# Kernel tuning notes

Measured on AMD Instinct MI355X. Metric: run time of the kernel, lower is better.

The kernel has to match this reference:

```python
import jax, jax.numpy as jnp
import numpy as np

N = 80000   # nodes
E = 320000  # directed edges
B = 3200    # graphs (25 nodes each)
D = 256     # emb_dim
L = 5       # num_layer
SIZES = [121, 8, 12, 15, 10, 9, 7, 3, 3]          # atom-feature vocab sizes
ESIZES = [25, 6, 2]                               # bond-feature vocab sizes
OFFS = np.concatenate([[0], np.cumsum(SIZES)[:-1]])  # offsets into fused node table
BN_EPS = 1e-5


def setup_inputs() -> dict:
    key = jax.random.key(0)
    ks = jax.random.split(key, 32)
    # int node features, per-column vocab bound
    x = jnp.stack([jax.random.randint(ks[i], (N,), 0, SIZES[i]) for i in range(9)], axis=1)
    edge_index = jax.random.randint(ks[9], (2, E), 0, N)
    edge_attr = jnp.stack([jax.random.randint(ks[10 + j], (E,), 0, ESIZES[j]) for j in range(3)], axis=1)
    batch = jnp.arange(N) // (N // B)  # sorted graph ids, 25 nodes per graph
    s = 0.1
    node_emb = jax.random.normal(ks[13], (int(sum(SIZES)), D)) * s  # fused 9 tables
    edge_emb1 = jax.random.normal(ks[14], (L, 25, D)) * s
    edge_emb2 = jax.random.normal(ks[15], (L, 6, D)) * s
    edge_emb3 = jax.random.normal(ks[16], (L, 2, D)) * s
    w = 0.05
    W1 = jax.random.normal(ks[17], (L, D, 2 * D)) * w
    b1 = jnp.zeros((L, 2 * D))
    W2 = jax.random.normal(ks[18], (L, 2 * D, D)) * w
    b2 = jnp.zeros((L, D))
    bn_g = jnp.ones((L, D))
    bn_b = jnp.zeros((L, D))
    H = D // 2
    HW1 = jax.random.normal(ks[19], (D, H)) * w
    Hb1 = jnp.zeros((H,))
    HW2 = jax.random.normal(ks[20], (H, H)) * w
    Hb2 = jnp.zeros((H,))
    HW3 = jax.random.normal(ks[21], (H, 2)) * w
    Hb3 = jnp.zeros((2,))
    return {"x": x, "edge_index": edge_index, "edge_attr": edge_attr, "batch": batch,
            "node_emb": node_emb, "edge_emb1": edge_emb1, "edge_emb2": edge_emb2,
            "edge_emb3": edge_emb3, "W1": W1, "b1": b1, "W2": W2, "b2": b2,
            "bn_g": bn_g, "bn_b": bn_b, "HW1": HW1, "Hb1": Hb1, "HW2": HW2,
            "Hb2": Hb2, "HW3": HW3, "Hb3": Hb3}


def _gnn_graphpred(x, edge_index, edge_attr, batch, node_emb, edge_emb1, edge_emb2,
                   edge_emb3, W1, b1, W2, b2, bn_g, bn_b, HW1, Hb1, HW2, Hb2, HW3, Hb3):
    n = x.shape[0]
    offs = jnp.asarray(OFFS, dtype=x.dtype)
    # sum of 9 atom embeddings == one gather into fused table
    h = node_emb[x + offs[None, :]].sum(axis=1)            # [N, D]
    # add self loops; self-loop edge_attr = [22, 0, 0]
    loop = jnp.arange(n, dtype=edge_index.dtype)
    src = jnp.concatenate([edge_index[0], loop])
    dst = jnp.concatenate([edge_index[1], loop])
    ea0 = jnp.concatenate([edge_attr[:, 0], jnp.full((n,), 22, edge_attr.dtype)])
    ea1 = jnp.concatenate([edge_attr[:, 1], jnp.zeros((n,), edge_attr.dtype)])
    ea2 = jnp.concatenate([edge_attr[:, 2], jnp.zeros((n,), edge_attr.dtype)])
    nl = W1.shape[0]
    relu_flag = jnp.arange(nl) < (nl - 1)   # ReLU on all but last layer (JK='last')

    def layer(hc, p):
        e1, e2, e3, w1, bb1, w2, bb2, g, b, flag = p
        eemb = e1[ea0] + e2[ea1] + e3[ea2]                 # [E+N, D]
        msg = hc[src] + eemb                                # gather + add
        aggr = jax.ops.segment_sum(msg, dst, num_segments=n)  # scatter-sum
        h2 = jax.nn.relu(aggr @ w1 + bb1) @ w2 + bb2        # GIN MLP
        mean = h2.mean(axis=0)
        var = h2.var(axis=0)                                # BatchNorm (batch stats)
        h2 = (h2 - mean) * jax.lax.rsqrt(var + BN_EPS) * g + b
        h2 = jnp.where(flag, jax.nn.relu(h2), h2)
        return h2, None

    h, _ = jax.lax.scan(layer, h, (edge_emb1, edge_emb2, edge_emb3, W1, b1, W2, b2,
                                   bn_g, bn_b, relu_flag))
    # super_node_rep: last node of each graph (batch is sorted)
    last_idx = jax.ops.segment_max(jnp.arange(n), batch, num_segments=B)
    super_rep = h[last_idx]                                 # [B, D]
    z = jax.nn.elu(super_rep @ HW1 + Hb1)
    z = jax.nn.elu(z @ HW2 + Hb2)
    return z @ HW3 + Hb3                                    # [B, 2]


def reference(x, edge_index, edge_attr, batch, node_emb, edge_emb1, edge_emb2,
              edge_emb3, W1, b1, W2, b2, bn_g, bn_b, HW1, Hb1, HW2, Hb2, HW3, Hb3):
    return _gnn_graphpred(x, edge_index, edge_attr, batch, node_emb, edge_emb1,
                          edge_emb2, edge_emb3, W1, b1, W2, b2, bn_g, bn_b,
                          HW1, Hb1, HW2, Hb2, HW3, Hb3)
```

## Files before the change

### kernel.cpp

```cpp
#include <hip/hip_runtime.h>
#include <hip/hip_bf16.h>

#define NN 80000
#define EE 320000
#define ET 400000
#define BB 3200
#define LL 5
#define NBLK 313
#define MLPB 1250

typedef __attribute__((ext_vector_type(8))) short bf16x8;
typedef __attribute__((ext_vector_type(8))) unsigned short u16x8;
typedef __attribute__((ext_vector_type(4))) float f32x4;

__device__ __forceinline__ float bf2f(unsigned short u) {
    unsigned int v = ((unsigned int)u) << 16;
    return __builtin_bit_cast(float, v);
}
__device__ __forceinline__ unsigned short f2bf(float f) {
    return __builtin_bit_cast(unsigned short, __float2bfloat16(f));
}

#define GLL16(SRC, DST) __builtin_amdgcn_global_load_lds( \
    (const __attribute__((address_space(1))) unsigned int*)(SRC), \
    (__attribute__((address_space(3))) unsigned int*)(DST), 16, 0, 0)


__global__ void k_deg(const int* ei, int* deg) {
    int e = blockIdx.x * 256 + threadIdx.x;
    if (e >= ET) return;
    int d = (e < EE) ? ei[EE + e] : (e - EE);
    atomicAdd(&deg[d], 1);
}

__global__ void k_scan1(const int* deg, int* blksum) {
    __shared__ int sh[256];
    int t = threadIdx.x, b = blockIdx.x;
    int i = b * 256 + t;
    int v = (i < NN) ? deg[i] : 0;
    sh[t] = v; __syncthreads();
    for (int off = 128; off > 0; off >>= 1) {
        if (t < off) sh[t] += sh[t + off];
        __syncthreads();
    }
    if (t == 0) blksum[b] = sh[0];
}

__global__ __launch_bounds__(512) void k_scan2(const int* blksum, int* blkoff) {
    __shared__ int sh[512];
    int t = threadIdx.x;
    int v = (t < NBLK) ? blksum[t] : 0;
    sh[t] = v; __syncthreads();
    for (int off = 1; off < 512; off <<= 1) {
        int x = (t >= off) ? sh[t - off] : 0;
        __syncthreads();
        sh[t] += x;
        __syncthreads();
    }
    if (t < NBLK) blkoff[t] = sh[t] - v;
}

__global__ void k_scan3(const int* deg, const int* blkoff, int* row_start, int* cursor) {
    __shared__ int sh[256];
    int t = threadIdx.x, b = blockIdx.x;
    int i = b * 256 + t;
    int v = (i < NN) ? deg[i] : 0;
    sh[t] = v; __syncthreads();
    for (int off = 1; off < 256; off <<= 1) {
        int x = (t >= off) ? sh[t - off] : 0;
        __syncthreads();
        sh[t] += x;
        __syncthreads();
    }
    int exc = sh[t] - v + blkoff[b];
    if (i < NN) { row_start[i] = exc; cursor[i] = exc; }
    if (i == NN - 1) row_start[NN] = exc + v;
}

__global__ void k_fill(const int* ei, const int* ea, int* cursor, int* eid, int* combo) {
    int e = blockIdx.x * 256 + threadIdx.x;
    if (e >= ET) return;
    int d = (e < EE) ? ei[EE + e] : (e - EE);
    int p = atomicAdd(&cursor[d], 1);
    eid[p] = e;
    int c;
    if (e < EE) c = ea[e * 3 + 0] * 12 + ea[e * 3 + 1] * 2 + ea[e * 3 + 2];
    else        c = 22 * 12;
    combo[e] = c;
}

__global__ void k_sortbkt(const int* row_start, int* eid) {
    int v = blockIdx.x * 256 + threadIdx.x;
    if (v >= NN) return;
    int s0 = row_start[v], s1 = row_start[v + 1];
    for (int i = s0 + 1; i < s1; i++) {
        int key = eid[i];
        int j = i - 1;
        while (j >= s0 && eid[j] > key) { eid[j + 1] = eid[j]; j--; }
        eid[j + 1] = key;
    }
}

__global__ void k_remap(const int* eid, const int* combo, const int* ei_src,
                        int* csrc, int* ccomb) {
    int p = blockIdx.x * 256 + threadIdx.x;
    if (p >= ET) return;
    int e = eid[p];
    csrc[p]  = (e < EE) ? ei_src[e] : (e - EE);
    ccomb[p] = combo[e];
}

__global__ void k_ecomb(const float* e1, const float* e2, const float* e3, float* ec) {
    int l = blockIdx.x / 300, c = blockIdx.x % 300, d = threadIdx.x;
    int a0 = c / 12, a1 = (c / 2) % 6, a2 = c & 1;
    ec[(size_t)(l * 300 + c) * 256 + d] =
        e1[(size_t)(l * 25 + a0) * 256 + d] +
        e2[(size_t)(l * 6 + a1) * 256 + d] +
        e3[(size_t)(l * 2 + a2) * 256 + d];
}

__global__ void k_w1t(const float* W, __hip_bfloat16* Whi, __hip_bfloat16* Wlo) {
    int i = blockIdx.x * 256 + threadIdx.x;
    if (i >= LL * 512 * 256) return;
    int l = i / (512 * 256); int r = i % (512 * 256); int n = r / 256; int k = r % 256;
    float w = W[(size_t)(l * 256 + k) * 512 + n];
    unsigned short hi = f2bf(w);
    Whi[i] = __float2bfloat16(w);
    Wlo[i] = __float2bfloat16(w - bf2f(hi));
}
__global__ void k_w2t(const float* W, __hip_bfloat16* Whi, __hip_bfloat16* Wlo) {
    int i = blockIdx.x * 256 + threadIdx.x;
    if (i >= LL * 256 * 512) return;
    int l = i / (256 * 512); int r = i % (256 * 512); int n = r / 512; int k = r % 512;
    float w = W[(size_t)(l * 512 + k) * 256 + n];
    unsigned short hi = f2bf(w);
    Whi[i] = __float2bfloat16(w);
    Wlo[i] = __float2bfloat16(w - bf2f(hi));
}

__global__ void k_nodeemb(const int* x, const float* emb, __hip_bfloat16* h) {
    const int offs[9] = {0, 121, 129, 141, 156, 166, 175, 182, 185};
    int i = blockIdx.x; int d = threadIdx.x;
    float acc = 0.f;
#pragma unroll
    for (int c = 0; c < 9; c++) {
        int idx = x[i * 9 + c] + offs[c];
        acc += emb[(size_t)idx * 256 + d];
    }
    h[(size_t)i * 256 + d] = __float2bfloat16(acc);
}


__global__ __launch_bounds__(256) void k_aggr(const __hip_bfloat16* h, const float* ecomb_l,
        const int* row_start, const int* csrc, const int* ccomb,
        __hip_bfloat16* aggrB) {
    int wid = threadIdx.x >> 6;
    int lane = threadIdx.x & 63;
    int v = blockIdx.x * 8 + wid * 2 + (lane >> 5);
    int sl = lane & 31;
    int s0 = row_start[v], s1 = row_start[v + 1];
    const unsigned short* hp = (const unsigned short*)h;
    float acc[8] = {0.f, 0.f, 0.f, 0.f, 0.f, 0.f, 0.f, 0.f};
    int p = s0;
    for (; p + 2 <= s1; p += 2) {
        int sA = csrc[p],     cA = ccomb[p];
        int sB = csrc[p + 1], cB = ccomb[p + 1];
        u16x8 hA = *(const u16x8*)(hp + (size_t)sA * 256 + sl * 8);
        u16x8 hB = *(const u16x8*)(hp + (size_t)sB * 256 + sl * 8);
        f32x4 eA0 = *(const f32x4*)(ecomb_l + (size_t)cA * 256 + sl * 8);
        f32x4 eA1 = *(const f32x4*)(ecomb_l + (size_t)cA * 256 + sl * 8 + 4);
        f32x4 eB0 = *(const f32x4*)(ecomb_l + (size_t)cB * 256 + sl * 8);
        f32x4 eB1 = *(const f32x4*)(ecomb_l + (size_t)cB * 256 + sl * 8 + 4);
        float tA[8] = { bf2f(hA[0]) + eA0.x, bf2f(hA[1]) + eA0.y,
                        bf2f(hA[2]) + eA0.z, bf2f(hA[3]) + eA0.w,
                        bf2f(hA[4]) + eA1.x, bf2f(hA[5]) + eA1.y,
                        bf2f(hA[6]) + eA1.z, bf2f(hA[7]) + eA1.w };
        float tB[8] = { bf2f(hB[0]) + eB0.x, bf2f(hB[1]) + eB0.y,
                        bf2f(hB[2]) + eB0.z, bf2f(hB[3]) + eB0.w,
                        bf2f(hB[4]) + eB1.x, bf2f(hB[5]) + eB1.y,
                        bf2f(hB[6]) + eB1.z, bf2f(hB[7]) + eB1.w };
#pragma unroll
        for (int j = 0; j < 8; j++) { acc[j] += tA[j]; acc[j] += tB[j]; }
    }
    if (p < s1) {
        int s = csrc[p], c = ccomb[p];
        u16x8 hv = *(const u16x8*)(hp + (size_t)s * 256 + sl * 8);
        f32x4 e0 = *(const f32x4*)(ecomb_l + (size_t)c * 256 + sl * 8);
        f32x4 e1 = *(const f32x4*)(ecomb_l + (size_t)c * 256 + sl * 8 + 4);
        acc[0] += bf2f(hv[0]) + e0.x;
        acc[1] += bf2f(hv[1]) + e0.y;
        acc[2] += bf2f(hv[2]) + e0.z;
        acc[3] += bf2f(hv[3]) + e0.w;
        acc[4] += bf2f(hv[4]) + e1.x;
        acc[5] += bf2f(hv[5]) + e1.y;
        acc[6] += bf2f(hv[6]) + e1.z;
        acc[7] += bf2f(hv[7]) + e1.w;
    }
    u16x8 o;
#pragma unroll
    for (int j = 0; j < 8; j++) o[j] = f2bf(acc[j]);
    *(u16x8*)((unsigned short*)aggrB + (size_t)v * 256 + sl * 8) = o;
}

template<bool LAST>
__global__ __launch_bounds__(512) void k_mlp(const __hip_bfloat16* aggrB,
        const __hip_bfloat16* W1hi, const __hip_bfloat16* W1lo, const float* b1v,
        const __hip_bfloat16* W2hi, const __hip_bfloat16* W2lo, const float* b2v,
        float* h2, float* psum, float* psq) {
    __shared__ __align__(16) char smem[160 * 1024];
    int tid = threadIdx.x;
    int wave = tid >> 6, lane = tid & 63;
    int lr = lane & 15, lk = lane >> 4;
    int mBase = blockIdx.x * 64;

    {
        const char* srcBase = (const char*)aggrB + (size_t)mBase * 512;
#pragma unroll
        for (int i = 0; i < 4; i++) {
            int g0 = wave * 4096 + i * 1024;
            int flat = g0 + lane * 16;
            int r = flat >> 9;
            int slot = (flat >> 4) & 31;
            int srcf = (r << 9) | (((slot ^ (r & 7)) & 31) << 4);
            GLL16(srcBase + srcf, smem + g0);
        }
    }

    const char* W1hB = (const char*)W1hi;
    const char* W1lB = (const char*)W1lo;
    auto stageW1 = [&](int buf, int k0) {
        char* dst = smem + 32768 + buf * 65536;
#pragma unroll
        for (int i = 0; i < 4; i++) {
            int g0 = i * 512 + wave * 64;
            int g  = g0 + lane;
            int n = g >> 2, j = g & 3;
            int ks = j ^ ((n + (n >> 2)) & 3);
            size_t so = (size_t)n * 512 + (size_t)k0 * 2 + ks * 16;
            GLL16(W1hB + so, dst + g0 * 16);
            GLL16(W1lB + so, dst + 32768 + g0 * 16);
        }
    };

    stageW1(0, 0);
    __syncthreads();

    f32x4 acc1[4][4] = {};
    for (int t = 0; t < 8; t++) {
        int cur = t & 1;
        if (t + 1 < 8) stageW1(cur ^ 1, (t + 1) * 32);
        const char* bW = smem + 32768 + cur * 65536;
        bf16x8 wh[4], wl[4], a[4];
#pragma unroll
        for (int n = 0; n < 4; n++) {
            int n0 = wave * 64 + n * 16 + lr;
            int go = (n0 * 4 + (lk ^ ((n0 + (n0 >> 2)) & 3))) * 16;
            wh[n] = *(const bf16x8*)(bW + go);
            wl[n] = *(const bf16x8*)(bW + 32768 + go);
        }
#pragma unroll
        for (int m = 0; m < 4; m++) {
            int r = m * 16 + lr;
            a[m] = *(const bf16x8*)(smem + r * 512 + ((((t * 4 + lk) ^ (r & 7)) & 31) * 16));
        }
#pragma unroll
        for (int m = 0; m < 4; m++)
#pragma unroll
            for (int n = 0; n < 4; n++) {
                acc1[m][n] = __builtin_amdgcn_mfma_f32_16x16x32_bf16(wh[n], a[m], acc1[m][n], 0, 0, 0);
                acc1[m][n] = __builtin_amdgcn_mfma_f32_16x16x32_bf16(wl[n], a[m], acc1[m][n], 0, 0, 0);
            }
        __syncthreads();
    }

    short* sAct = (short*)smem;
#pragma unroll
    for (int n = 0; n < 4; n++) {
        int col0 = wave * 64 + n * 16 + lk * 4;
        f32x4 bi = *(const f32x4*)(b1v + col0);
        int cb = col0 >> 3, ci = col0 & 7;
#pragma unroll
        for (int m = 0; m < 4; m++) {
            int row = m * 16 + lr;
            short4 o;
            o.x = (short)f2bf(fmaxf(acc1[m][n][0] + bi.x, 0.f));
            o.y = (short)f2bf(fmaxf(acc1[m][n][1] + bi.y, 0.f));
            o.z = (short)f2bf(fmaxf(acc1[m][n][2] + bi.z, 0.f));
            o.w = (short)f2bf(fmaxf(acc1[m][n][3] + bi.w, 0.f));
            *(short4*)(&sAct[row * 512 + (((cb ^ (row & 7)) << 3) | ci)]) = o;
        }
    }

    const char* W2hB = (const char*)W2hi;
    const char* W2lB = (const char*)W2lo;
    auto stageW2 = [&](int buf, int k0) {
        char* dst = smem + 65536 + buf * 32768;
#pragma unroll
        for (int i = 0; i < 2; i++) {
            int g0 = i * 512 + wave * 64;
            int g  = g0 + lane;
            int n = g >> 2, j = g & 3;
            int ks = j ^ ((n + (n >> 2)) & 3);
            size_t so = (size_t)n * 1024 + (size_t)k0 * 2 + ks * 16;
            GLL16(W2hB + so, dst + g0 * 16);
            GLL16(W2lB + so, dst + 16384 + g0 * 16);
        }
    };
    stageW2(0, 0);
    __syncthreads();

    f32x4 acc2[4][2] = {};
    for (int t = 0; t < 16; t++) {
        int cur = t & 1;
        if (t + 1 < 16) stageW2(cur ^ 1, (t + 1) * 32);
        const char* bW = smem + 65536 + cur * 32768;
        bf16x8 a2[4], w2h[2], w2l[2];
        int kb = t * 4 + lk;
#pragma unroll
        for (int m = 0; m < 4; m++) {
            int row = m * 16 + lr;
            a2[m] = *(const bf16x8*)((const char*)sAct + row * 1024 + (((kb ^ (row & 7)) & 63) << 4));
        }
#pragma unroll
        for (int n = 0; n < 2; n++) {
            int n0 = wave * 32 + n * 16 + lr;
            int go = (n0 * 4 + (lk ^ ((n0 + (n0 >> 2)) & 3))) * 16;
            w2h[n] = *(const bf16x8*)(bW + go);
            w2l[n] = *(const bf16x8*)(bW + 16384 + go);
        }
#pragma unroll
        for (int m = 0; m < 4; m++)
#pragma unroll
            for (int n = 0; n < 2; n++) {
                acc2[m][n] = __builtin_amdgcn_mfma_f32_16x16x32_bf16(a2[m], w2h[n], acc2[m][n], 0, 0, 0);
                acc2[m][n] = __builtin_amdgcn_mfma_f32_16x16x32_bf16(a2[m], w2l[n], acc2[m][n], 0, 0, 0);
            }
        __syncthreads();
    }

    float colS[2] = {0.f, 0.f}, colQ[2] = {0.f, 0.f};
#pragma unroll
    for (int m = 0; m < 4; m++)
#pragma unroll
        for (int n = 0; n < 2; n++) {
            int col = wave * 32 + n * 16 + lr;
            float bi = b2v[col];
#pragma unroll
            for (int j = 0; j < 4; j++) {
                int row = mBase + m * 16 + lk * 4 + j;
                float v = acc2[m][n][j] + bi;
                colS[n] += v; colQ[n] += v * v;
                if (!LAST || (row % 25 == 24))
                    h2[(size_t)row * 256 + col] = v;
            }
        }
#pragma unroll
    for (int n = 0; n < 2; n++) {
        colS[n] += __shfl_xor(colS[n], 16);
        colQ[n] += __shfl_xor(colQ[n], 16);
        colS[n] += __shfl_xor(colS[n], 32);
        colQ[n] += __shfl_xor(colQ[n], 32);
    }
    if (lk == 0) {
#pragma unroll
        for (int n = 0; n < 2; n++) {
            int col = wave * 32 + n * 16 + lr;
            psum[(size_t)col * MLPB + blockIdx.x] = colS[n];
            psq [(size_t)col * MLPB + blockIdx.x] = colQ[n];
        }
    }
}

__global__ __launch_bounds__(256) void k_bn2(const float* psum, const float* psq,
                                             const float* g, const float* bta, float* stat) {
    __shared__ float s1[256], s2[256];
    int d = blockIdx.x; int t = threadIdx.x;
    float a = 0.f, b = 0.f;
    for (int rb = t; rb < MLPB; rb += 256) {
        a += psum[(size_t)d * MLPB + rb];
        b += psq [(size_t)d * MLPB + rb];
    }
    s1[t] = a; s2[t] = b; __syncthreads();
    for (int off = 128; off > 0; off >>= 1) {
        if (t < off) { s1[t] += s1[t + off]; s2[t] += s2[t + off]; }
        __syncthreads();
    }
    if (t == 0) {
        float mean = s1[0] / NN;
        float var = s2[0] / NN - mean * mean;
        float sc = rsqrtf(var + 1e-5f) * g[d];
        stat[d] = sc;
        stat[256 + d] = bta[d] - mean * sc;
    }
}

__global__ void k_bnapply(const float* h2, const float* stat, __hip_bfloat16* h, int relu) {
    int i = (blockIdx.x * 256 + threadIdx.x) * 4;
    int d = i & 255;
    f32x4 v = *(const f32x4*)(h2 + i);
    f32x4 sc = *(const f32x4*)(stat + d);
    f32x4 sh = *(const f32x4*)(stat + 256 + d);
    float r0 = v.x * sc.x + sh.x;
    float r1 = v.y * sc.y + sh.y;
    float r2 = v.z * sc.z + sh.z;
    float r3 = v.w * sc.w + sh.w;
    if (relu) {
        r0 = fmaxf(r0, 0.f); r1 = fmaxf(r1, 0.f);
        r2 = fmaxf(r2, 0.f); r3 = fmaxf(r3, 0.f);
    }
    ushort4 o;
    o.x = f2bf(r0); o.y = f2bf(r1); o.z = f2bf(r2); o.w = f2bf(r3);
    *(ushort4*)((unsigned short*)h + i) = o;
}

__global__ __launch_bounds__(128) void k_head(const float* h2, const float* stat,
        const float* HW1, const float* Hb1, const float* HW2, const float* Hb2,
        const float* HW3, const float* Hb3, float* out) {
    __shared__ float row[256], z1[128], z2[128];
    int g = blockIdx.x; int t = threadIdx.x;
    size_t node = (size_t)g * 25 + 24;
    row[t]       = h2[node * 256 + t] * stat[t] + stat[256 + t];
    row[t + 128] = h2[node * 256 + t + 128] * stat[t + 128] + stat[256 + t + 128];
    __syncthreads();
    float acc = Hb1[t];
    for (int k = 0; k < 256; k++) acc += row[k] * HW1[k * 128 + t];
    z1[t] = acc > 0.f ? acc : expm1f(acc);
    __syncthreads();
    acc = Hb2[t];
    for (int k = 0; k < 128; k++) acc += z1[k] * HW2[k * 128 + t];
    z2[t] = acc > 0.f ? acc : expm1f(acc);
    __syncthreads();
    if (t < 2) {
        acc = Hb3[t];
        for (int k = 0; k < 128; k++) acc += z2[k] * HW3[k * 2 + t];
        out[g * 2 + t] = acc;
    }
}


extern "C" void kernel_launch(void* const* d_in, const int* in_sizes, int n_in,
                              void* d_out, int out_size, void* d_ws, size_t ws_size,
                              hipStream_t stream) {
    const int* x          = (const int*)d_in[0];
    const int* edge_index = (const int*)d_in[1];
    const int* edge_attr  = (const int*)d_in[2];
    const float* node_emb = (const float*)d_in[4];
    const float* ee1 = (const float*)d_in[5];
    const float* ee2 = (const float*)d_in[6];
    const float* ee3 = (const float*)d_in[7];
    const float* W1  = (const float*)d_in[8];
    const float* b1  = (const float*)d_in[9];
    const float* W2  = (const float*)d_in[10];
    const float* b2  = (const float*)d_in[11];
    const float* bng = (const float*)d_in[12];
    const float* bnb = (const float*)d_in[13];
    const float* HW1 = (const float*)d_in[14];
    const float* Hb1 = (const float*)d_in[15];
    const float* HW2 = (const float*)d_in[16];
    const float* Hb2 = (const float*)d_in[17];
    const float* HW3 = (const float*)d_in[18];
    const float* Hb3 = (const float*)d_in[19];
    float* out = (float*)d_out;

    char* ws = (char*)d_ws;
    size_t off = 0;
    auto alloc = [&](size_t bytes) -> char* {
        off = (off + 255) & ~(size_t)255;
        char* p = ws + off;
        off += bytes;
        return p;
    };
    int* deg       = (int*)alloc((size_t)NN * 4);
    int* cursor    = (int*)alloc((size_t)NN * 4);
    int* row_start = (int*)alloc((size_t)(NN + 1) * 4);
    int* blksum    = (int*)alloc((size_t)(NBLK + 1) * 4);
    int* blkoff    = (int*)alloc((size_t)(NBLK + 1) * 4);
    int* eid       = (int*)alloc((size_t)ET * 4);
    int* combo     = (int*)alloc((size_t)ET * 4);
    int* csrc      = (int*)alloc((size_t)ET * 4);
    int* ccomb     = (int*)alloc((size_t)ET * 4);
    float* ecomb   = (float*)alloc((size_t)LL * 300 * 256 * 4);
    __hip_bfloat16* W1hi = (__hip_bfloat16*)alloc((size_t)LL * 512 * 256 * 2);
    __hip_bfloat16* W1lo = (__hip_bfloat16*)alloc((size_t)LL * 512 * 256 * 2);
    __hip_bfloat16* W2hi = (__hip_bfloat16*)alloc((size_t)LL * 256 * 512 * 2);
    __hip_bfloat16* W2lo = (__hip_bfloat16*)alloc((size_t)LL * 256 * 512 * 2);
    __hip_bfloat16* h    = (__hip_bfloat16*)alloc((size_t)NN * 256 * 2);
    __hip_bfloat16* aggrB = (__hip_bfloat16*)alloc((size_t)NN * 256 * 2);
    float* h2     = (float*)alloc((size_t)NN * 256 * 4);
    float* psum   = (float*)alloc((size_t)256 * MLPB * 4);
    float* psq    = (float*)alloc((size_t)256 * MLPB * 4);
    float* bnstat = (float*)alloc((size_t)512 * 4);

    hipMemsetAsync(deg, 0, (size_t)NN * 4, stream);
    k_deg<<<(ET + 255) / 256, 256, 0, stream>>>(edge_index, deg);
    k_scan1<<<NBLK, 256, 0, stream>>>(deg, blksum);
    k_scan2<<<1, 512, 0, stream>>>(blksum, blkoff);
    k_scan3<<<NBLK, 256, 0, stream>>>(deg, blkoff, row_start, cursor);
    k_fill<<<(ET + 255) / 256, 256, 0, stream>>>(edge_index, edge_attr, cursor, eid, combo);
    k_sortbkt<<<(NN + 255) / 256, 256, 0, stream>>>(row_start, eid);
    k_remap<<<(ET + 255) / 256, 256, 0, stream>>>(eid, combo, edge_index, csrc, ccomb);
    k_ecomb<<<LL * 300, 256, 0, stream>>>(ee1, ee2, ee3, ecomb);
    k_w1t<<<(LL * 512 * 256 + 255) / 256, 256, 0, stream>>>(W1, W1hi, W1lo);
    k_w2t<<<(LL * 256 * 512 + 255) / 256, 256, 0, stream>>>(W2, W2hi, W2lo);
    k_nodeemb<<<NN, 256, 0, stream>>>(x, node_emb, h);

    for (int l = 0; l < LL; l++) {
        k_aggr<<<NN / 8, 256, 0, stream>>>(h, ecomb + (size_t)l * 300 * 256, row_start,
                                           csrc, ccomb, aggrB);
        if (l < LL - 1) {
            k_mlp<false><<<MLPB, 512, 0, stream>>>(aggrB,
                W1hi + (size_t)l * 512 * 256, W1lo + (size_t)l * 512 * 256, b1 + l * 512,
                W2hi + (size_t)l * 256 * 512, W2lo + (size_t)l * 256 * 512, b2 + l * 256,
                h2, psum, psq);
        } else {
            k_mlp<true><<<MLPB, 512, 0, stream>>>(aggrB,
                W1hi + (size_t)l * 512 * 256, W1lo + (size_t)l * 512 * 256, b1 + l * 512,
                W2hi + (size_t)l * 256 * 512, W2lo + (size_t)l * 256 * 512, b2 + l * 256,
                h2, psum, psq);
        }
        k_bn2<<<256, 256, 0, stream>>>(psum, psq, bng + l * 256, bnb + l * 256, bnstat);
        if (l < LL - 1)
            k_bnapply<<<NN * 256 / (256 * 4), 256, 0, stream>>>(h2, bnstat, h, 1);
    }

    k_head<<<BB, 128, 0, stream>>>(h2, bnstat, HW1, Hb1, HW2, Hb2, HW3, Hb3, out);
}
```

Before: 1.109 ms.

## Double MLP row tile to 128 and stage hi/lo weights in alternating phases

Each MLP block now handles 128 rows instead of 64, so each staged weight tile feeds twice as many MFMAs and total weight traffic is halved. The hi and lo weight halves are now staged separately in alternating pipeline phases, with activation fragments held in registers across each pair, which keeps shared memory within the 160KB budget. The cost is more accumulator registers (launch bounds set to one block per CU), half as many blocks (625), and twice as many barrier-separated pipeline steps.

```diff
diff --git a/kernel.cpp b/kernel.cpp
--- a/kernel.cpp
+++ b/kernel.cpp
@@ -7,7 +7,7 @@
 #define BB 3200
 #define LL 5
 #define NBLK 313
-#define MLPB 1250
+#define MLPB 625
 
 typedef __attribute__((ext_vector_type(8))) short bf16x8;
 typedef __attribute__((ext_vector_type(8))) unsigned short u16x8;
@@ -203,7 +203,7 @@
 }
 
 template<bool LAST>
-__global__ __launch_bounds__(512) void k_mlp(const __hip_bfloat16* aggrB,
+__global__ __launch_bounds__(512, 1) void k_mlp(const __hip_bfloat16* aggrB,
         const __hip_bfloat16* W1hi, const __hip_bfloat16* W1lo, const float* b1v,
         const __hip_bfloat16* W2hi, const __hip_bfloat16* W2lo, const float* b2v,
         float* h2, float* psum, float* psq) {
@@ -211,13 +211,13 @@
     int tid = threadIdx.x;
     int wave = tid >> 6, lane = tid & 63;
     int lr = lane & 15, lk = lane >> 4;
-    int mBase = blockIdx.x * 64;
+    int mBase = blockIdx.x * 128;
 
     {
         const char* srcBase = (const char*)aggrB + (size_t)mBase * 512;
 #pragma unroll
-        for (int i = 0; i < 4; i++) {
-            int g0 = wave * 4096 + i * 1024;
+        for (int i = 0; i < 8; i++) {
+            int g0 = wave * 8192 + i * 1024;
             int flat = g0 + lane * 16;
             int r = flat >> 9;
             int slot = (flat >> 4) & 31;
@@ -226,134 +226,147 @@
         }
     }
 
-    const char* W1hB = (const char*)W1hi;
-    const char* W1lB = (const char*)W1lo;
-    auto stageW1 = [&](int buf, int k0) {
-        char* dst = smem + 32768 + buf * 65536;
+    auto stageW1 = [&](int buf, int k, const char* Wsel) {
+        char* dst = smem + 65536 + buf * 32768;
 #pragma unroll
         for (int i = 0; i < 4; i++) {
             int g0 = i * 512 + wave * 64;
             int g  = g0 + lane;
             int n = g >> 2, j = g & 3;
             int ks = j ^ ((n + (n >> 2)) & 3);
-            size_t so = (size_t)n * 512 + (size_t)k0 * 2 + ks * 16;
-            GLL16(W1hB + so, dst + g0 * 16);
-            GLL16(W1lB + so, dst + 32768 + g0 * 16);
+            size_t so = (size_t)n * 512 + (size_t)k * 64 + ks * 16;
+            GLL16(Wsel + so, dst + g0 * 16);
         }
     };
-
-    stageW1(0, 0);
+    const char* W1sel[2] = { (const char*)W1hi, (const char*)W1lo };
+    stageW1(0, 0, W1sel[0]);
     __syncthreads();
 
-    f32x4 acc1[4][4] = {};
-    for (int t = 0; t < 8; t++) {
-        int cur = t & 1;
-        if (t + 1 < 8) stageW1(cur ^ 1, (t + 1) * 32);
-        const char* bW = smem + 32768 + cur * 65536;
-        bf16x8 wh[4], wl[4], a[4];
+    f32x4 acc1[2][4][4] = {};
+    bf16x8 aF[2][4];
+    for (int p = 0; p < 16; p++) {
+        int cur = p & 1;
+        if (p + 1 < 16) stageW1(cur ^ 1, (p + 1) >> 1, W1sel[(p + 1) & 1]);
+        const char* bW = smem + 65536 + cur * 32768;
+        int k = p >> 1, sel = p & 1;
+        bf16x8 w[4];
 #pragma unroll
         for (int n = 0; n < 4; n++) {
             int n0 = wave * 64 + n * 16 + lr;
             int go = (n0 * 4 + (lk ^ ((n0 + (n0 >> 2)) & 3))) * 16;
-            wh[n] = *(const bf16x8*)(bW + go);
-            wl[n] = *(const bf16x8*)(bW + 32768 + go);
-        }
-#pragma unroll
-        for (int m = 0; m < 4; m++) {
-            int r = m * 16 + lr;
-            a[m] = *(const bf16x8*)(smem + r * 512 + ((((t * 4 + lk) ^ (r & 7)) & 31) * 16));
-        }
-#pragma unroll
-        for (int m = 0; m < 4; m++)
-#pragma unroll
-            for (int n = 0; n < 4; n++) {
-                acc1[m][n] = __builtin_amdgcn_mfma_f32_16x16x32_bf16(wh[n], a[m], acc1[m][n], 0, 0, 0);
-                acc1[m][n] = __builtin_amdgcn_mfma_f32_16x16x32_bf16(wl[n], a[m], acc1[m][n], 0, 0, 0);
+            w[n] = *(const bf16x8*)(bW + go);
+        }
+        if (sel == 0) {
+#pragma unroll
+            for (int T = 0; T < 2; T++)
+#pragma unroll
+                for (int m = 0; m < 4; m++) {
+                    int r = T * 64 + m * 16 + lr;
+                    aF[T][m] = *(const bf16x8*)(smem + r * 512 +
+                               ((((k * 4 + lk) ^ (r & 7)) & 31) * 16));
+                }
+        }
+#pragma unroll
+        for (int T = 0; T < 2; T++)
+#pragma unroll
+            for (int m = 0; m < 4; m++)
+#pragma unroll
+                for (int n = 0; n < 4; n++)
+                    acc1[T][m][n] = __builtin_amdgcn_mfma_f32_16x16x32_bf16(
+                        w[n], aF[T][m], acc1[T][m][n], 0, 0, 0);
+        __syncthreads();
+    }
+
+    short* sAct = (short*)smem;
+#pragma unroll
+    for (int T = 0; T < 2; T++)
+#pragma unroll
+        for (int n = 0; n < 4; n++) {
+            int col0 = wave * 64 + n * 16 + lk * 4;
+            f32x4 bi = *(const f32x4*)(b1v + col0);
+            int cb = col0 >> 3, ci = col0 & 7;
+#pragma unroll
+            for (int m = 0; m < 4; m++) {
+                int row = T * 64 + m * 16 + lr;
+                short4 o;
+                o.x = (short)f2bf(fmaxf(acc1[T][m][n][0] + bi.x, 0.f));
+                o.y = (short)f2bf(fmaxf(acc1[T][m][n][1] + bi.y, 0.f));
+                o.z = (short)f2bf(fmaxf(acc1[T][m][n][2] + bi.z, 0.f));
+                o.w = (short)f2bf(fmaxf(acc1[T][m][n][3] + bi.w, 0.f));
+                *(short4*)(&sAct[row * 512 + (((cb ^ (row & 7)) << 3) | ci)]) = o;
             }
-        __syncthreads();
-    }
-
-    short* sAct = (short*)smem;
-#pragma unroll
-    for (int n = 0; n < 4; n++) {
-        int col0 = wave * 64 + n * 16 + lk * 4;
-        f32x4 bi = *(const f32x4*)(b1v + col0);
-        int cb = col0 >> 3, ci = col0 & 7;
-#pragma unroll
-        for (int m = 0; m < 4; m++) {
-            int row = m * 16 + lr;
-            short4 o;
-            o.x = (short)f2bf(fmaxf(acc1[m][n][0] + bi.x, 0.f));
-            o.y = (short)f2bf(fmaxf(acc1[m][n][1] + bi.y, 0.f));
-            o.z = (short)f2bf(fmaxf(acc1[m][n][2] + bi.z, 0.f));
-            o.w = (short)f2bf(fmaxf(acc1[m][n][3] + bi.w, 0.f));
-            *(short4*)(&sAct[row * 512 + (((cb ^ (row & 7)) << 3) | ci)]) = o;
-        }
-    }
-
-    const char* W2hB = (const char*)W2hi;
-    const char* W2lB = (const char*)W2lo;
-    auto stageW2 = [&](int buf, int k0) {
-        char* dst = smem + 65536 + buf * 32768;
+        }
+
+    auto stageW2 = [&](int buf, int k, const char* Wsel) {
+        char* dst = smem + 131072 + buf * 16384;
 #pragma unroll
         for (int i = 0; i < 2; i++) {
             int g0 = i * 512 + wave * 64;
             int g  = g0 + lane;
             int n = g >> 2, j = g & 3;
             int ks = j ^ ((n + (n >> 2)) & 3);
-            size_t so = (size_t)n * 1024 + (size_t)k0 * 2 + ks * 16;
-            GLL16(W2hB + so, dst + g0 * 16);
-            GLL16(W2lB + so, dst + 16384 + g0 * 16);
+            size_t so = (size_t)n * 1024 + (size_t)k * 64 + ks * 16;
+            GLL16(Wsel + so, dst + g0 * 16);
         }
     };
-    stageW2(0, 0);
+    const char* W2sel[2] = { (const char*)W2hi, (const char*)W2lo };
+    stageW2(0, 0, W2sel[0]);
     __syncthreads();
 
-    f32x4 acc2[4][2] = {};
-    for (int t = 0; t < 16; t++) {
-        int cur = t & 1;
-        if (t + 1 < 16) stageW2(cur ^ 1, (t + 1) * 32);
-        const char* bW = smem + 65536 + cur * 32768;
-        bf16x8 a2[4], w2h[2], w2l[2];
-        int kb = t * 4 + lk;
-#pragma unroll
-        for (int m = 0; m < 4; m++) {
-            int row = m * 16 + lr;
-            a2[m] = *(const bf16x8*)((const char*)sAct + row * 1024 + (((kb ^ (row & 7)) & 63) << 4));
-        }
+    f32x4 acc2[2][4][2] = {};
+    bf16x8 a2F[2][4];
+    for (int p = 0; p < 32; p++) {
+        int cur = p & 1;
+        if (p + 1 < 32) stageW2(cur ^ 1, (p + 1) >> 1, W2sel[(p + 1) & 1]);
+        const char* bW = smem + 131072 + cur * 16384;
+        int k = p >> 1, sel = p & 1;
+        bf16x8 w[2];
 #pragma unroll
         for (int n = 0; n < 2; n++) {
             int n0 = wave * 32 + n * 16 + lr;
             int go = (n0 * 4 + (lk ^ ((n0 + (n0 >> 2)) & 3))) * 16;
-            w2h[n] = *(const bf16x8*)(bW + go);
-            w2l[n] = *(const bf16x8*)(bW + 16384 + go);
-        }
+            w[n] = *(const bf16x8*)(bW + go);
+        }
+        if (sel == 0) {
+            int kb = k * 4 + lk;
+#pragma unroll
+            for (int T = 0; T < 2; T++)
+#pragma unroll
+                for (int m = 0; m < 4; m++) {
+                    int row = T * 64 + m * 16 + lr;
+                    a2F[T][m] = *(const bf16x8*)((const char*)sAct + row * 1024 +
+                                (((kb ^ (row & 7)) & 63) << 4));
+                }
+        }
+#pragma unroll
+        for (int T = 0; T < 2; T++)
+#pragma unroll
+            for (int m = 0; m < 4; m++)
+#pragma unroll
+                for (int n = 0; n < 2; n++)
+                    acc2[T][m][n] = __builtin_amdgcn_mfma_f32_16x16x32_bf16(
+                        a2F[T][m], w[n], acc2[T][m][n], 0, 0, 0);
+        __syncthreads();
+    }
+
+    float colS[2] = {0.f, 0.f}, colQ[2] = {0.f, 0.f};
+#pragma unroll
+    for (int T = 0; T < 2; T++)
 #pragma unroll
         for (int m = 0; m < 4; m++)
 #pragma unroll
             for (int n = 0; n < 2; n++) {
-                acc2[m][n] = __builtin_amdgcn_mfma_f32_16x16x32_bf16(a2[m], w2h[n], acc2[m][n], 0, 0, 0);
-                acc2[m][n] = __builtin_amdgcn_mfma_f32_16x16x32_bf16(a2[m], w2l[n], acc2[m][n], 0, 0, 0);
+                int col = wave * 32 + n * 16 + lr;
+                float bi = b2v[col];
+#pragma unroll
+                for (int j = 0; j < 4; j++) {
+                    int row = mBase + T * 64 + m * 16 + lk * 4 + j;
+                    float v = acc2[T][m][n][j] + bi;
+                    colS[n] += v; colQ[n] += v * v;
+                    if (!LAST || (row % 25 == 24))
+                        h2[(size_t)row * 256 + col] = v;
+                }
             }
-        __syncthreads();
-    }
-
-    float colS[2] = {0.f, 0.f}, colQ[2] = {0.f, 0.f};
-#pragma unroll
-    for (int m = 0; m < 4; m++)
-#pragma unroll
-        for (int n = 0; n < 2; n++) {
-            int col = wave * 32 + n * 16 + lr;
-            float bi = b2v[col];
-#pragma unroll
-            for (int j = 0; j < 4; j++) {
-                int row = mBase + m * 16 + lk * 4 + j;
-                float v = acc2[m][n][j] + bi;
-                colS[n] += v; colQ[n] += v * v;
-                if (!LAST || (row % 25 == 24))
-                    h2[(size_t)row * 256 + col] = v;
-            }
-        }
 #pragma unroll
     for (int n = 0; n < 2; n++) {
         colS[n] += __shfl_xor(colS[n], 16);
```

New measurement: 988.7 us. 10.8% less time.
